# Kernel tuning notes

Hardware: AMD Instinct MI355X
Metric: run time of the kernel (lower is better)

## Reference

```python
import jax, jax.numpy as jnp
import numpy as np

B, N, IDIM, ODIM = 4096, 32, 1024, 1024


def setup_inputs() -> dict:
    key = jax.random.key(0)
    k1, k2, k3 = jax.random.split(key, 3)
    x = jax.random.normal(k1, (B, IDIM), dtype=jnp.float32)
    weight = jax.random.normal(k2, (N, ODIM, IDIM), dtype=jnp.float32)
    gate_w = jax.random.normal(k3, (N, IDIM), dtype=jnp.float32) * (1.0 / np.sqrt(IDIM))
    gate_b = jnp.zeros((N,), dtype=jnp.float32)
    return {"x": x, "weight": weight, "gate_w": gate_w, "gate_b": gate_b}


def reference(x, weight, gate_w, gate_b):
    # per-expert projection: [b, n, odim] (the large intermediate the torch code
    # materializes via einsum 'noi,biz->bnoz' with z=1)
    y = jnp.einsum('noi,bi->bno', weight, x)
    # gate weights: gelu(Linear(idim -> n)) ; torch gelu default is exact (erf)
    g = jax.nn.gelu(x @ gate_w.T + gate_b, approximate=False)  # [b, n]
    # gated combine over experts (the `y @ g` step after rearrange)
    out = jnp.einsum('bno,bn->bo', y, g)  # [b, odim]
    return out
```

## Files before the change

kernel.cpp:

```cpp
#include <hip/hip_runtime.h>
#include <hip/hip_bf16.h>
#include <math.h>


#define BSZ  4096
#define NEXP 32
#define IDIM 1024
#define ODIM 1024

typedef __attribute__((ext_vector_type(8))) short bf16x8;
typedef __attribute__((ext_vector_type(4))) float f32x4;

#define GLOAD_LDS16(g, l) __builtin_amdgcn_global_load_lds( \
    (const __attribute__((address_space(1))) void*)(g),     \
    (__attribute__((address_space(3))) void*)(l), 16, 0, 0)

#define SBAR __builtin_amdgcn_sched_barrier(0)
#define WAITV6 do { asm volatile("s_waitcnt vmcnt(6)" ::: "memory"); SBAR; } while (0)
#define WAITV0 do { asm volatile("s_waitcnt vmcnt(0)" ::: "memory"); SBAR; } while (0)
#define WAITL0 do { asm volatile("s_waitcnt lgkmcnt(0)" ::: "memory"); SBAR; } while (0)
#define BARRIER do { __builtin_amdgcn_s_barrier(); SBAR; } while (0)

__device__ __forceinline__ unsigned short f2bf(float f) {
  unsigned u = __float_as_uint(f);
  unsigned r = (u + 0x7FFFu + ((u >> 16) & 1u)) >> 16;
  return (unsigned short)r;
}

__global__ void zero_kernel(float* __restrict__ out) {
  int i = blockIdx.x * blockDim.x + threadIdx.x;
  ((float4*)out)[i] = make_float4(0.f, 0.f, 0.f, 0.f);
}

__global__ void conv_kernel(const float* __restrict__ in, unsigned short* __restrict__ outb) {
  int i = blockIdx.x * blockDim.x + threadIdx.x;
  const float4* p = (const float4*)in + (size_t)i * 2;
  float4 a = p[0], b = p[1];
  union { bf16x8 v; unsigned short s[8]; } o;
  o.s[0] = f2bf(a.x); o.s[1] = f2bf(a.y); o.s[2] = f2bf(a.z); o.s[3] = f2bf(a.w);
  o.s[4] = f2bf(b.x); o.s[5] = f2bf(b.y); o.s[6] = f2bf(b.z); o.s[7] = f2bf(b.w);
  ((bf16x8*)outb)[i] = o.v;
}

__global__ void gate_kernel(const float* __restrict__ x, const float* __restrict__ gw,
                            const float* __restrict__ gb, float* __restrict__ gT) {
  const int lane = threadIdx.x & 63;
  const int row = blockIdx.x * 4 + (threadIdx.x >> 6);
  const float4* xr = (const float4*)(x + (size_t)row * IDIM);
  float4 xv[4];
#pragma unroll
  for (int t = 0; t < 4; ++t) xv[t] = xr[t * 64 + lane];
  for (int n = 0; n < NEXP; ++n) {
    const float4* wr = (const float4*)(gw + (size_t)n * IDIM);
    float s = 0.f;
#pragma unroll
    for (int t = 0; t < 4; ++t) {
      float4 wv = wr[t * 64 + lane];
      s += xv[t].x * wv.x + xv[t].y * wv.y + xv[t].z * wv.z + xv[t].w * wv.w;
    }
#pragma unroll
    for (int off = 32; off > 0; off >>= 1) s += __shfl_down(s, off, 64);
    if (lane == 0) {
      float v = s + gb[n];
      gT[(size_t)n * BSZ + row] = 0.5f * v * (1.0f + erff(v * 0.70710678118f));
    }
  }
}

__global__ __launch_bounds__(512, 2) void gemm_kernel(
    const unsigned short* __restrict__ xb,
    const unsigned short* __restrict__ wb,
    const float* __restrict__ gT,
    float* __restrict__ out)
{
  __shared__ unsigned short As[3][256 * 64];
  __shared__ unsigned short Bs[3][128 * 64];
  __shared__ float g_lds[16][256];

  const int tid  = threadIdx.x;
  const int lane = tid & 63;
  const int wid  = tid >> 6;
  const int wm   = wid >> 1;
  const int wn   = wid & 1;

  const int orig  = blockIdx.x;
  const int wgid  = (orig & 7) * 32 + (orig >> 3);
  const int mtile = wgid & 15;
  const int grp   = wgid >> 4;
  const int split = grp & 1;
  const int col0  = (grp >> 1) * 128;
  const int row0  = mtile * 256;

  const int srow = lane >> 3;
  const int jsrc = (lane & 7) ^ srow;
  size_t a_off[4], b_off[2];
#pragma unroll
  for (int l = 0; l < 4; ++l)
    a_off[l] = (size_t)(row0 + (wid * 4 + l) * 8 + srow) * IDIM + jsrc * 8;
#pragma unroll
  for (int l = 0; l < 2; ++l)
    b_off[l] = (size_t)(col0 + (wid * 2 + l) * 8 + srow) * IDIM + jsrc * 8;

  const int frow = lane & 15;
  const int hi   = lane >> 4;

  f32x4 acc[4][4], acc_e[4][4];
#pragma unroll
  for (int i = 0; i < 4; ++i)
#pragma unroll
    for (int j = 0; j < 4; ++j) {
      acc[i][j]   = f32x4{0.f, 0.f, 0.f, 0.f};
      acc_e[i][j] = f32x4{0.f, 0.f, 0.f, 0.f};
    }

  {
    const int e = tid >> 5;
    const int r = (tid & 31) * 8;
    const float* src = gT + ((size_t)(split * 16 + e) << 12) + row0 + r;
    *(float4*)&g_lds[e][r]     = *(const float4*)src;
    *(float4*)&g_lds[e][r + 4] = *(const float4*)(src + 4);
  }

  auto STAGE_H = [&](int buf, int kt, int half) {
    const int e  = kt >> 4;
    const int i0 = (kt & 15) << 6;
    const unsigned short* wb_n = wb + ((size_t)(split * 16 + e) << 20);
#pragma unroll
    for (int l = half * 2; l < half * 2 + 2; ++l)
      GLOAD_LDS16(xb + a_off[l] + i0, &As[buf][(wid * 4 + l) * 512]);
    GLOAD_LDS16(wb_n + b_off[half] + i0, &Bs[buf][(wid * 2 + half) * 512]);
  };

  __syncthreads();
  STAGE_H(0, 0, 0); STAGE_H(0, 0, 1);
  STAGE_H(1, 1, 0); STAGE_H(1, 1, 1);
  WAITV6;
  BARRIER;

  int cur = 0;
#pragma unroll 1
  for (int kt = 0; kt < 256; ++kt) {
    int sbuf = cur + 2; if (sbuf >= 3) sbuf -= 3;
    const unsigned short* A_ = &As[cur][0];
    const unsigned short* B_ = &Bs[cur][0];
    const int g0 = hi ^ (frow & 7);
    const int g1 = (4 + hi) ^ (frow & 7);

    bf16x8 af0[4], bf0[4];
#pragma unroll
    for (int ni = 0; ni < 4; ++ni)
      bf0[ni] = *(const bf16x8*)&B_[(wn * 64 + ni * 16 + frow) * 64 + g0 * 8];
#pragma unroll
    for (int mi = 0; mi < 4; ++mi)
      af0[mi] = *(const bf16x8*)&A_[(wm * 64 + mi * 16 + frow) * 64 + g0 * 8];
    if (kt < 254) STAGE_H(sbuf, kt + 2, 0);
    BARRIER;
    WAITL0;
    __builtin_amdgcn_s_setprio(1);
#pragma unroll
    for (int mi = 0; mi < 4; ++mi)
#pragma unroll
      for (int ni = 0; ni < 4; ++ni)
        acc_e[mi][ni] = __builtin_amdgcn_mfma_f32_16x16x32_bf16(
            af0[mi], bf0[ni], acc_e[mi][ni], 0, 0, 0);
    __builtin_amdgcn_s_setprio(0);
    BARRIER;

    bf16x8 af1[4], bf1[4];
#pragma unroll
    for (int ni = 0; ni < 4; ++ni)
      bf1[ni] = *(const bf16x8*)&B_[(wn * 64 + ni * 16 + frow) * 64 + g1 * 8];
#pragma unroll
    for (int mi = 0; mi < 4; ++mi)
      af1[mi] = *(const bf16x8*)&A_[(wm * 64 + mi * 16 + frow) * 64 + g1 * 8];
    if (kt < 254) STAGE_H(sbuf, kt + 2, 1);
    if (kt < 254) { WAITV6; } else if (kt == 254) { WAITV0; }
    BARRIER;
    WAITL0;
    __builtin_amdgcn_s_setprio(1);
#pragma unroll
    for (int mi = 0; mi < 4; ++mi)
#pragma unroll
      for (int ni = 0; ni < 4; ++ni)
        acc_e[mi][ni] = __builtin_amdgcn_mfma_f32_16x16x32_bf16(
            af1[mi], bf1[ni], acc_e[mi][ni], 0, 0, 0);
    __builtin_amdgcn_s_setprio(0);

    if ((kt & 15) == 15) {
      const int e = kt >> 4;
#pragma unroll
      for (int mi = 0; mi < 4; ++mi) {
        float4 gv = *(const float4*)&g_lds[e][wm * 64 + mi * 16 + hi * 4];
        f32x4 g4 = f32x4{gv.x, gv.y, gv.z, gv.w};
#pragma unroll
        for (int ni = 0; ni < 4; ++ni) {
          acc[mi][ni] += g4 * acc_e[mi][ni];
          acc_e[mi][ni] = f32x4{0.f, 0.f, 0.f, 0.f};
        }
      }
    }
    BARRIER;
    if (++cur == 3) cur = 0;
  }

  const int orow0 = row0 + wm * 64 + hi * 4;
  const int ocol0 = col0 + wn * 64 + frow;
#pragma unroll
  for (int mi = 0; mi < 4; ++mi)
#pragma unroll
    for (int j = 0; j < 4; ++j) {
      const int r = orow0 + mi * 16 + j;
#pragma unroll
      for (int ni = 0; ni < 4; ++ni)
        atomicAdd(out + (size_t)r * ODIM + ocol0 + ni * 16, acc[mi][ni][j]);
    }
}

extern "C" void kernel_launch(void* const* d_in, const int* in_sizes, int n_in,
                              void* d_out, int out_size, void* d_ws, size_t ws_size,
                              hipStream_t stream) {
  const float* x  = (const float*)d_in[0];
  const float* w  = (const float*)d_in[1];
  const float* gw = (const float*)d_in[2];
  const float* gb = (const float*)d_in[3];
  float* out = (float*)d_out;

  unsigned short* xb   = (unsigned short*)d_ws;
  unsigned short* wbuf = (unsigned short*)((char*)d_ws + (8u << 20));
  float*          gT   = (float*)((char*)d_ws + (72u << 20));

  zero_kernel<<<(BSZ * ODIM / 4) / 256, 256, 0, stream>>>(out);
  conv_kernel<<<(BSZ * IDIM / 8) / 256, 256, 0, stream>>>(x, xb);
  conv_kernel<<<(NEXP * ODIM * IDIM / 8) / 256, 256, 0, stream>>>(w, wbuf);
  gate_kernel<<<BSZ / 4, 256, 0, stream>>>(x, gw, gb, gT);

  gemm_kernel<<<256, 512, 0, stream>>>(xb, wbuf, gT, out);
}
```

Measured before the change: 347.6 us.

## Simplify GEMM main loop to one barrier per k-tile with full-tile staging

Replaces the ping-pong schedule (four barriers per k-step, split half-stage loads, setprio around MFMA clusters) with a simpler loop: wait for the current tile's loads, take one barrier, issue the whole next-next tile's loads, then run both MFMA halves. This removes barrier overhead and explicit lgkmcnt waits, leaving the compiler to interleave LDS reads and MFMAs. In exchange it loses the two-wave-per-SIMD ping-pong priority scheduling, and the triple buffer with a single barrier has to stay race-free. With every load for a tile now issued at once, the vmcnt(6) wait still matches one outstanding stage.

Result: slower. 419.7 us (+20.7%).

```diff
diff --git a/kernel.cpp b/kernel.cpp
--- a/kernel.cpp
+++ b/kernel.cpp
@@ -16,10 +16,8 @@
     (__attribute__((address_space(3))) void*)(l), 16, 0, 0)
 
 #define SBAR __builtin_amdgcn_sched_barrier(0)
-#define WAITV6 do { asm volatile("s_waitcnt vmcnt(6)" ::: "memory"); SBAR; } while (0)
-#define WAITV0 do { asm volatile("s_waitcnt vmcnt(0)" ::: "memory"); SBAR; } while (0)
-#define WAITL0 do { asm volatile("s_waitcnt lgkmcnt(0)" ::: "memory"); SBAR; } while (0)
-#define BARRIER do { __builtin_amdgcn_s_barrier(); SBAR; } while (0)
+#define WAITV6 asm volatile("s_waitcnt vmcnt(6)" ::: "memory")
+#define WAITV0 asm volatile("s_waitcnt vmcnt(0)" ::: "memory")
 
 __device__ __forceinline__ unsigned short f2bf(float f) {
   unsigned u = __float_as_uint(f);
@@ -121,26 +119,32 @@
     *(float4*)&g_lds[e][r + 4] = *(const float4*)(src + 4);
   }
 
-  auto STAGE_H = [&](int buf, int kt, int half) {
+  auto STAGE = [&](int buf, int kt) {
     const int e  = kt >> 4;
     const int i0 = (kt & 15) << 6;
     const unsigned short* wb_n = wb + ((size_t)(split * 16 + e) << 20);
 #pragma unroll
-    for (int l = half * 2; l < half * 2 + 2; ++l)
+    for (int l = 0; l < 4; ++l)
       GLOAD_LDS16(xb + a_off[l] + i0, &As[buf][(wid * 4 + l) * 512]);
-    GLOAD_LDS16(wb_n + b_off[half] + i0, &Bs[buf][(wid * 2 + half) * 512]);
+#pragma unroll
+    for (int l = 0; l < 2; ++l)
+      GLOAD_LDS16(wb_n + b_off[l] + i0, &Bs[buf][(wid * 2 + l) * 512]);
   };
 
   __syncthreads();
-  STAGE_H(0, 0, 0); STAGE_H(0, 0, 1);
-  STAGE_H(1, 1, 0); STAGE_H(1, 1, 1);
-  WAITV6;
-  BARRIER;
+  STAGE(0, 0);
+  STAGE(1, 1);
 
   int cur = 0;
 #pragma unroll 1
   for (int kt = 0; kt < 256; ++kt) {
-    int sbuf = cur + 2; if (sbuf >= 3) sbuf -= 3;
+    if (kt == 255) { WAITV0; } else { WAITV6; }
+    SBAR;
+    __builtin_amdgcn_s_barrier();
+    SBAR;
+
+    if (kt < 254) { int s = cur + 2; if (s >= 3) s -= 3; STAGE(s, kt + 2); }
+
     const unsigned short* A_ = &As[cur][0];
     const unsigned short* B_ = &Bs[cur][0];
     const int g0 = hi ^ (frow & 7);
@@ -153,18 +157,12 @@
 #pragma unroll
     for (int mi = 0; mi < 4; ++mi)
       af0[mi] = *(const bf16x8*)&A_[(wm * 64 + mi * 16 + frow) * 64 + g0 * 8];
-    if (kt < 254) STAGE_H(sbuf, kt + 2, 0);
-    BARRIER;
-    WAITL0;
-    __builtin_amdgcn_s_setprio(1);
 #pragma unroll
     for (int mi = 0; mi < 4; ++mi)
 #pragma unroll
       for (int ni = 0; ni < 4; ++ni)
         acc_e[mi][ni] = __builtin_amdgcn_mfma_f32_16x16x32_bf16(
             af0[mi], bf0[ni], acc_e[mi][ni], 0, 0, 0);
-    __builtin_amdgcn_s_setprio(0);
-    BARRIER;
 
     bf16x8 af1[4], bf1[4];
 #pragma unroll
@@ -173,18 +171,12 @@
 #pragma unroll
     for (int mi = 0; mi < 4; ++mi)
       af1[mi] = *(const bf16x8*)&A_[(wm * 64 + mi * 16 + frow) * 64 + g1 * 8];
-    if (kt < 254) STAGE_H(sbuf, kt + 2, 1);
-    if (kt < 254) { WAITV6; } else if (kt == 254) { WAITV0; }
-    BARRIER;
-    WAITL0;
-    __builtin_amdgcn_s_setprio(1);
 #pragma unroll
     for (int mi = 0; mi < 4; ++mi)
 #pragma unroll
       for (int ni = 0; ni < 4; ++ni)
         acc_e[mi][ni] = __builtin_amdgcn_mfma_f32_16x16x32_bf16(
             af1[mi], bf1[ni], acc_e[mi][ni], 0, 0, 0);
-    __builtin_amdgcn_s_setprio(0);
 
     if ((kt & 15) == 15) {
       const int e = kt >> 4;
@@ -199,7 +191,6 @@
         }
       }
     }
-    BARRIER;
     if (++cur == 3) cur = 0;
   }
 
```

## Fold gate into pre-scaled bf16 activations and run one concatenated-K GEMM

Applied to the files above, without the earlier changes.

Instead of accumulating each expert's product separately and then applying the gate weight per expert, a new scale_kernel writes per-expert copies of x already multiplied by the gate value, in bf16. The GEMM then runs as a single reduction over expert×idim. It also moves to 256x256 tiles with double buffering, 4 expert splits, and chunked launches sized to the available workspace. This removes the per-expert epilogue and the extra accumulator registers. In exchange it materializes a very large scaled-activation buffer (up to 32 copies of x), adding substantial HBM write and read traffic, and it rounds g*x to bf16.

New measurement: 464.8 us. +33.7%, slower.

```diff
diff --git a/kernel.cpp b/kernel.cpp
--- a/kernel.cpp
+++ b/kernel.cpp
@@ -8,6 +8,7 @@
 #define IDIM 1024
 #define ODIM 1024
 
+typedef unsigned short u16;
 typedef __attribute__((ext_vector_type(8))) short bf16x8;
 typedef __attribute__((ext_vector_type(4))) float f32x4;
 
@@ -16,15 +17,13 @@
     (__attribute__((address_space(3))) void*)(l), 16, 0, 0)
 
 #define SBAR __builtin_amdgcn_sched_barrier(0)
-#define WAITV6 do { asm volatile("s_waitcnt vmcnt(6)" ::: "memory"); SBAR; } while (0)
-#define WAITV0 do { asm volatile("s_waitcnt vmcnt(0)" ::: "memory"); SBAR; } while (0)
+#define WAITV0 asm volatile("s_waitcnt vmcnt(0)" ::: "memory")
 #define WAITL0 do { asm volatile("s_waitcnt lgkmcnt(0)" ::: "memory"); SBAR; } while (0)
 #define BARRIER do { __builtin_amdgcn_s_barrier(); SBAR; } while (0)
 
-__device__ __forceinline__ unsigned short f2bf(float f) {
+__device__ __forceinline__ u16 f2bf(float f) {
   unsigned u = __float_as_uint(f);
-  unsigned r = (u + 0x7FFFu + ((u >> 16) & 1u)) >> 16;
-  return (unsigned short)r;
+  return (u16)((u + 0x7FFFu + ((u >> 16) & 1u)) >> 16);
 }
 
 __global__ void zero_kernel(float* __restrict__ out) {
@@ -32,11 +31,11 @@
   ((float4*)out)[i] = make_float4(0.f, 0.f, 0.f, 0.f);
 }
 
-__global__ void conv_kernel(const float* __restrict__ in, unsigned short* __restrict__ outb) {
+__global__ void conv_kernel(const float* __restrict__ in, u16* __restrict__ outb) {
   int i = blockIdx.x * blockDim.x + threadIdx.x;
   const float4* p = (const float4*)in + (size_t)i * 2;
   float4 a = p[0], b = p[1];
-  union { bf16x8 v; unsigned short s[8]; } o;
+  union { bf16x8 v; u16 s[8]; } o;
   o.s[0] = f2bf(a.x); o.s[1] = f2bf(a.y); o.s[2] = f2bf(a.z); o.s[3] = f2bf(a.w);
   o.s[4] = f2bf(b.x); o.s[5] = f2bf(b.y); o.s[6] = f2bf(b.z); o.s[7] = f2bf(b.w);
   ((bf16x8*)outb)[i] = o.v;
@@ -67,146 +66,160 @@
   }
 }
 
+__global__ void scale_kernel(const float* __restrict__ x, const float* __restrict__ gT,
+                             u16* __restrict__ xs, int base) {
+  int idx = blockIdx.x * 256 + threadIdx.x;
+  int chunk = idx & 127;
+  int b = (idx >> 7) & 4095;
+  int e = idx >> 19;
+  const float4* xp = (const float4*)(x + ((size_t)b << 10) + chunk * 8);
+  float4 v0 = xp[0], v1 = xp[1];
+  float g = gT[((size_t)(base + e) << 12) + b];
+  union { bf16x8 v; u16 s[8]; } o;
+  o.s[0] = f2bf(g * v0.x); o.s[1] = f2bf(g * v0.y);
+  o.s[2] = f2bf(g * v0.z); o.s[3] = f2bf(g * v0.w);
+  o.s[4] = f2bf(g * v1.x); o.s[5] = f2bf(g * v1.y);
+  o.s[6] = f2bf(g * v1.z); o.s[7] = f2bf(g * v1.w);
+  *(bf16x8*)&xs[((size_t)e << 22) + ((size_t)b << 10) + chunk * 8] = o.v;
+}
+
 __global__ __launch_bounds__(512, 2) void gemm_kernel(
-    const unsigned short* __restrict__ xb,
-    const unsigned short* __restrict__ wb,
-    const float* __restrict__ gT,
-    float* __restrict__ out)
+    const u16* __restrict__ xs,
+    const u16* __restrict__ wb,
+    float* __restrict__ out,
+    int eps)
 {
-  __shared__ unsigned short As[3][256 * 64];
-  __shared__ unsigned short Bs[3][128 * 64];
-  __shared__ float g_lds[16][256];
+  __shared__ u16 As[2][256 * 64];
+  __shared__ u16 Bs[2][256 * 64];
 
   const int tid  = threadIdx.x;
   const int lane = tid & 63;
   const int wid  = tid >> 6;
-  const int wm   = wid >> 1;
-  const int wn   = wid & 1;
+  const int wm   = wid >> 2;
+  const int wn   = wid & 3;
 
   const int orig  = blockIdx.x;
   const int wgid  = (orig & 7) * 32 + (orig >> 3);
   const int mtile = wgid & 15;
   const int grp   = wgid >> 4;
-  const int split = grp & 1;
-  const int col0  = (grp >> 1) * 128;
+  const int split = grp & 3;
+  const int col0  = (grp >> 2) * 256;
   const int row0  = mtile * 256;
 
   const int srow = lane >> 3;
   const int jsrc = (lane & 7) ^ srow;
-  size_t a_off[4], b_off[2];
-#pragma unroll
-  for (int l = 0; l < 4; ++l)
-    a_off[l] = (size_t)(row0 + (wid * 4 + l) * 8 + srow) * IDIM + jsrc * 8;
-#pragma unroll
-  for (int l = 0; l < 2; ++l)
-    b_off[l] = (size_t)(col0 + (wid * 2 + l) * 8 + srow) * IDIM + jsrc * 8;
+  size_t a_off[4], b_off[4];
+#pragma unroll
+  for (int l = 0; l < 4; ++l) {
+    a_off[l] = ((size_t)(row0 + (wid * 4 + l) * 8 + srow) << 10) + jsrc * 8;
+    b_off[l] = ((size_t)(col0 + (wid * 4 + l) * 8 + srow) << 10) + jsrc * 8;
+  }
 
   const int frow = lane & 15;
   const int hi   = lane >> 4;
-
-  f32x4 acc[4][4], acc_e[4][4];
-#pragma unroll
-  for (int i = 0; i < 4; ++i)
-#pragma unroll
-    for (int j = 0; j < 4; ++j) {
-      acc[i][j]   = f32x4{0.f, 0.f, 0.f, 0.f};
-      acc_e[i][j] = f32x4{0.f, 0.f, 0.f, 0.f};
-    }
-
-  {
-    const int e = tid >> 5;
-    const int r = (tid & 31) * 8;
-    const float* src = gT + ((size_t)(split * 16 + e) << 12) + row0 + r;
-    *(float4*)&g_lds[e][r]     = *(const float4*)src;
-    *(float4*)&g_lds[e][r + 4] = *(const float4*)(src + 4);
-  }
-
-  auto STAGE_H = [&](int buf, int kt, int half) {
-    const int e  = kt >> 4;
-    const int i0 = (kt & 15) << 6;
-    const unsigned short* wb_n = wb + ((size_t)(split * 16 + e) << 20);
-#pragma unroll
-    for (int l = half * 2; l < half * 2 + 2; ++l)
-      GLOAD_LDS16(xb + a_off[l] + i0, &As[buf][(wid * 4 + l) * 512]);
-    GLOAD_LDS16(wb_n + b_off[half] + i0, &Bs[buf][(wid * 2 + half) * 512]);
+  const int g0 = hi ^ (frow & 7);
+  const int g1 = (4 + hi) ^ (frow & 7);
+  const int arow = (wm * 128 + frow) * 64;
+  const int brow = (wn * 64 + frow) * 64;
+
+  f32x4 acc[8][4];
+#pragma unroll
+  for (int i = 0; i < 8; ++i)
+#pragma unroll
+    for (int j = 0; j < 4; ++j) acc[i][j] = f32x4{0.f, 0.f, 0.f, 0.f};
+
+  auto SA = [&](int buf, int kt, int l) {
+    const int e = split * eps + (kt >> 4);
+    const size_t i0 = (size_t)((kt & 15) << 6);
+    GLOAD_LDS16(xs + ((size_t)e << 22) + a_off[l] + i0, &As[buf][(wid * 4 + l) * 512]);
   };
-
-  __syncthreads();
-  STAGE_H(0, 0, 0); STAGE_H(0, 0, 1);
-  STAGE_H(1, 1, 0); STAGE_H(1, 1, 1);
-  WAITV6;
+  auto SB = [&](int buf, int kt, int l) {
+    const int e = split * eps + (kt >> 4);
+    const size_t i0 = (size_t)((kt & 15) << 6);
+    GLOAD_LDS16(wb + ((size_t)e << 20) + b_off[l] + i0, &Bs[buf][(wid * 4 + l) * 512]);
+  };
+
+  const int NKT = eps << 4;
+
+#pragma unroll
+  for (int l = 0; l < 4; ++l) { SA(0, 0, l); SB(0, 0, l); }
+  WAITV0;
   BARRIER;
 
   int cur = 0;
 #pragma unroll 1
-  for (int kt = 0; kt < 256; ++kt) {
-    int sbuf = cur + 2; if (sbuf >= 3) sbuf -= 3;
-    const unsigned short* A_ = &As[cur][0];
-    const unsigned short* B_ = &Bs[cur][0];
-    const int g0 = hi ^ (frow & 7);
-    const int g1 = (4 + hi) ^ (frow & 7);
-
-    bf16x8 af0[4], bf0[4];
-#pragma unroll
-    for (int ni = 0; ni < 4; ++ni)
-      bf0[ni] = *(const bf16x8*)&B_[(wn * 64 + ni * 16 + frow) * 64 + g0 * 8];
-#pragma unroll
-    for (int mi = 0; mi < 4; ++mi)
-      af0[mi] = *(const bf16x8*)&A_[(wm * 64 + mi * 16 + frow) * 64 + g0 * 8];
-    if (kt < 254) STAGE_H(sbuf, kt + 2, 0);
-    BARRIER;
-    WAITL0;
-    __builtin_amdgcn_s_setprio(1);
-#pragma unroll
-    for (int mi = 0; mi < 4; ++mi)
-#pragma unroll
-      for (int ni = 0; ni < 4; ++ni)
-        acc_e[mi][ni] = __builtin_amdgcn_mfma_f32_16x16x32_bf16(
-            af0[mi], bf0[ni], acc_e[mi][ni], 0, 0, 0);
-    __builtin_amdgcn_s_setprio(0);
-    BARRIER;
-
-    bf16x8 af1[4], bf1[4];
-#pragma unroll
-    for (int ni = 0; ni < 4; ++ni)
-      bf1[ni] = *(const bf16x8*)&B_[(wn * 64 + ni * 16 + frow) * 64 + g1 * 8];
-#pragma unroll
-    for (int mi = 0; mi < 4; ++mi)
-      af1[mi] = *(const bf16x8*)&A_[(wm * 64 + mi * 16 + frow) * 64 + g1 * 8];
-    if (kt < 254) STAGE_H(sbuf, kt + 2, 1);
-    if (kt < 254) { WAITV6; } else if (kt == 254) { WAITV0; }
-    BARRIER;
-    WAITL0;
-    __builtin_amdgcn_s_setprio(1);
-#pragma unroll
-    for (int mi = 0; mi < 4; ++mi)
-#pragma unroll
-      for (int ni = 0; ni < 4; ++ni)
-        acc_e[mi][ni] = __builtin_amdgcn_mfma_f32_16x16x32_bf16(
-            af1[mi], bf1[ni], acc_e[mi][ni], 0, 0, 0);
-    __builtin_amdgcn_s_setprio(0);
-
-    if ((kt & 15) == 15) {
-      const int e = kt >> 4;
-#pragma unroll
-      for (int mi = 0; mi < 4; ++mi) {
-        float4 gv = *(const float4*)&g_lds[e][wm * 64 + mi * 16 + hi * 4];
-        f32x4 g4 = f32x4{gv.x, gv.y, gv.z, gv.w};
-#pragma unroll
-        for (int ni = 0; ni < 4; ++ni) {
-          acc[mi][ni] += g4 * acc_e[mi][ni];
-          acc_e[mi][ni] = f32x4{0.f, 0.f, 0.f, 0.f};
-        }
-      }
-    }
-    BARRIER;
-    if (++cur == 3) cur = 0;
-  }
-
-  const int orow0 = row0 + wm * 64 + hi * 4;
+  for (int kt = 0; kt < NKT; ++kt) {
+    const u16* A_ = &As[cur][0];
+    const u16* B_ = &Bs[cur][0];
+    const int nb = cur ^ 1;
+    const bool pf = (kt + 1 < NKT);
+
+    bf16x8 bA[4], a0[4];
+#pragma unroll
+    for (int ni = 0; ni < 4; ++ni) bA[ni] = *(const bf16x8*)&B_[brow + ni * 1024 + g0 * 8];
+#pragma unroll
+    for (int mi = 0; mi < 4; ++mi) a0[mi] = *(const bf16x8*)&A_[arow + mi * 1024 + g0 * 8];
+    if (pf) { SA(nb, kt + 1, 0); SA(nb, kt + 1, 1); SB(nb, kt + 1, 0); }
+    BARRIER; WAITL0;
+    __builtin_amdgcn_s_setprio(1);
+#pragma unroll
+    for (int mi = 0; mi < 4; ++mi)
+#pragma unroll
+      for (int ni = 0; ni < 4; ++ni)
+        acc[mi][ni] = __builtin_amdgcn_mfma_f32_16x16x32_bf16(a0[mi], bA[ni], acc[mi][ni], 0, 0, 0);
+    __builtin_amdgcn_s_setprio(0);
+    BARRIER;
+
+    bf16x8 a1[4];
+#pragma unroll
+    for (int mi = 0; mi < 4; ++mi) a1[mi] = *(const bf16x8*)&A_[arow + (mi + 4) * 1024 + g0 * 8];
+    if (pf) { SA(nb, kt + 1, 2); SA(nb, kt + 1, 3); SB(nb, kt + 1, 1); }
+    BARRIER; WAITL0;
+    __builtin_amdgcn_s_setprio(1);
+#pragma unroll
+    for (int mi = 0; mi < 4; ++mi)
+#pragma unroll
+      for (int ni = 0; ni < 4; ++ni)
+        acc[mi + 4][ni] = __builtin_amdgcn_mfma_f32_16x16x32_bf16(a1[mi], bA[ni], acc[mi + 4][ni], 0, 0, 0);
+    __builtin_amdgcn_s_setprio(0);
+    BARRIER;
+
+    bf16x8 bB[4], a2[4];
+#pragma unroll
+    for (int ni = 0; ni < 4; ++ni) bB[ni] = *(const bf16x8*)&B_[brow + ni * 1024 + g1 * 8];
+#pragma unroll
+    for (int mi = 0; mi < 4; ++mi) a2[mi] = *(const bf16x8*)&A_[arow + mi * 1024 + g1 * 8];
+    if (pf) { SB(nb, kt + 1, 2); SB(nb, kt + 1, 3); }
+    BARRIER; WAITL0;
+    __builtin_amdgcn_s_setprio(1);
+#pragma unroll
+    for (int mi = 0; mi < 4; ++mi)
+#pragma unroll
+      for (int ni = 0; ni < 4; ++ni)
+        acc[mi][ni] = __builtin_amdgcn_mfma_f32_16x16x32_bf16(a2[mi], bB[ni], acc[mi][ni], 0, 0, 0);
+    __builtin_amdgcn_s_setprio(0);
+    BARRIER;
+
+    bf16x8 a3[4];
+#pragma unroll
+    for (int mi = 0; mi < 4; ++mi) a3[mi] = *(const bf16x8*)&A_[arow + (mi + 4) * 1024 + g1 * 8];
+    BARRIER; WAITL0;
+    __builtin_amdgcn_s_setprio(1);
+#pragma unroll
+    for (int mi = 0; mi < 4; ++mi)
+#pragma unroll
+      for (int ni = 0; ni < 4; ++ni)
+        acc[mi + 4][ni] = __builtin_amdgcn_mfma_f32_16x16x32_bf16(a3[mi], bB[ni], acc[mi + 4][ni], 0, 0, 0);
+    __builtin_amdgcn_s_setprio(0);
+    if (pf) WAITV0;
+    BARRIER;
+    cur ^= 1;
+  }
+
+  const int orow0 = row0 + wm * 128 + hi * 4;
   const int ocol0 = col0 + wn * 64 + frow;
 #pragma unroll
-  for (int mi = 0; mi < 4; ++mi)
+  for (int mi = 0; mi < 8; ++mi)
 #pragma unroll
     for (int j = 0; j < 4; ++j) {
       const int r = orow0 + mi * 16 + j;
@@ -225,14 +238,23 @@
   const float* gb = (const float*)d_in[3];
   float* out = (float*)d_out;
 
-  unsigned short* xb   = (unsigned short*)d_ws;
-  unsigned short* wbuf = (unsigned short*)((char*)d_ws + (8u << 20));
-  float*          gT   = (float*)((char*)d_ws + (72u << 20));
+  const size_t MiB = 1u << 20;
+  int EPR;
+  if      (ws_size >= 321 * MiB) EPR = 32;
+  else if (ws_size >=  81 * MiB) EPR = 8;
+  else                           EPR = 4;
+  const int NR = NEXP / EPR;
+
+  u16*   xs   = (u16*)d_ws;
+  u16*   wbuf = (u16*)((char*)d_ws + (size_t)EPR * 8 * MiB);
+  float* gT   = (float*)((char*)d_ws + (size_t)EPR * 10 * MiB);
 
   zero_kernel<<<(BSZ * ODIM / 4) / 256, 256, 0, stream>>>(out);
-  conv_kernel<<<(BSZ * IDIM / 8) / 256, 256, 0, stream>>>(x, xb);
-  conv_kernel<<<(NEXP * ODIM * IDIM / 8) / 256, 256, 0, stream>>>(w, wbuf);
   gate_kernel<<<BSZ / 4, 256, 0, stream>>>(x, gw, gb, gT);
 
-  gemm_kernel<<<256, 512, 0, stream>>>(xb, wbuf, gT, out);
-}
+  for (int r = 0; r < NR; ++r) {
+    conv_kernel<<<EPR * 512, 256, 0, stream>>>(w + (size_t)r * EPR * IDIM * ODIM, wbuf);
+    scale_kernel<<<EPR * 2048, 256, 0, stream>>>(x, gT, xs, r * EPR);
+    gemm_kernel<<<256, 512, 0, stream>>>(xs, wbuf, out, EPR / 4);
+  }
+}
```
